# Performance work log

Measured on AMD Instinct MI355X. Metric: run time of the kernel, lower is better.

Reference implementation:

```python
import jax, jax.numpy as jnp
import numpy as np

B, L, D = 2048, 64, 128
NODES = 512
EPS = 1e-6


def setup_inputs() -> dict:
    key = jax.random.key(0)
    ks = jax.random.split(key, 9)
    src_ids = jax.random.randint(ks[0], (B, L), 0, NODES, dtype=jnp.int32)
    dst_ids = jax.random.randint(ks[1], (B, L), 0, NODES, dtype=jnp.int32)
    src_node_ids = jax.random.randint(ks[2], (B,), 1, NODES, dtype=jnp.int32)
    dst_node_ids = jax.random.randint(ks[3], (B,), 1, NODES, dtype=jnp.int32)
    node_interact_times = 100.0 + jax.random.uniform(ks[4], (B,), jnp.float32)
    src_times = jax.random.uniform(ks[5], (B, L), jnp.float32) * 100.0
    dst_times = jax.random.uniform(ks[6], (B, L), jnp.float32) * 100.0
    W1 = jax.random.normal(ks[7], (1, D), jnp.float32) * 0.5
    b1 = jnp.zeros((D,), jnp.float32)
    W2 = jax.random.normal(ks[8], (D, D), jnp.float32) * (1.0 / np.sqrt(D))
    b2 = jnp.zeros((D,), jnp.float32)
    return dict(src_padded_nodes_neighbor_ids=src_ids,
                dst_padded_nodes_neighbor_ids=dst_ids,
                src_node_ids=src_node_ids, dst_node_ids=dst_node_ids,
                node_interact_times=node_interact_times,
                src_padded_nodes_neighbor_times=src_times,
                dst_padded_nodes_neighbor_times=dst_times,
                W1=W1, b1=b1, W2=W2, b2=b2)


def _group_stats(ids, t):
    # per-position stats of the group sharing the same neighbor id. ids,t: (L,)
    n_pos = ids.shape[0]
    eq = ids[:, None] == ids[None, :]                       # (L,L) group membership
    n = eq.sum(1)                                           # group size at each position
    nf = n.astype(t.dtype)
    tb = jnp.broadcast_to(t[None, :], (n_pos, n_pos))
    tmax = jnp.max(jnp.where(eq, tb, -jnp.inf), axis=1)
    tmin = jnp.min(jnp.where(eq, tb, jnp.inf), axis=1)
    # mean(diff(sorted(ts))) == (max-min)/(n-1)
    avg_iat = jnp.where(n > 1, (tmax - tmin) / jnp.maximum(nf - 1.0, 1.0), 0.0)
    # stable rank of each element inside its own group (order statistic)
    pos = jnp.arange(n_pos)
    before = (t[:, None] < t[None, :]) | ((t[:, None] == t[None, :]) & (pos[:, None] < pos[None, :]))
    rank = jnp.sum(eq & before, axis=0)
    split = n // 2
    sel = eq & (rank[None, :] == split[:, None])            # exactly one per group
    t_split = jnp.sum(jnp.where(sel, tb, 0.0), axis=1)      # sorted(ts)[n//2]
    denom = jnp.maximum(nf - split.astype(t.dtype) - 1.0, 1.0)
    recent_iat = jnp.where(n >= 4, (tmax - t_split) / denom, 0.0)
    valid = ids != 0                                        # dicts skip neighbor id 0
    return nf, jnp.where(valid, avg_iat, 0.0), jnp.where(valid, recent_iat, 0.0)


def _cross_lookup(ids_a, ids_b, vals_b):
    # dict.get(nid, 0.0) over the other side's per-group values (id 0 excluded)
    match = (ids_a[:, None] == ids_b[None, :]) & (ids_b[None, :] != 0)
    idx = jnp.argmax(match, axis=1)
    return jnp.where(match.any(1), vals_b[idx], 0.0)


def _last_time(ids_a, ids_b, t_b):
    # dict comprehension keeps the LAST occurrence's timestamp (id 0 excluded)
    match = (ids_a[:, None] == ids_b[None, :]) & (ids_b[None, :] != 0)
    score = jnp.where(match, jnp.arange(ids_b.shape[0])[None, :], -1)
    li = score.max(1)
    return jnp.where(li >= 0, t_b[jnp.maximum(li, 0)], 0.0)


def _side_features(ids_a, t_a, ids_b, t_b, other_node_id, cur_t,
                   n_a, avg_a, rec_a, avg_b, rec_b, other_first):
    ft = t_a.dtype
    c_self = n_a
    c_other = jnp.sum(ids_a[:, None] == ids_b[None, :], axis=1).astype(ft)
    is_other = (ids_a == other_node_id).astype(ft)
    connects = (c_other > 0).astype(ft)
    freq_asym = jnp.where(c_other > 0, c_self / (c_other + EPS), 0.0)
    rcy_self = cur_t - t_a
    rcy_other = cur_t - _last_time(ids_a, ids_b, t_b)
    temp_asym = jnp.where(rcy_self > EPS, rcy_other / (rcy_self + EPS), 0.0)
    iat_other = _cross_lookup(ids_a, ids_b, avg_b)
    iat_asym = jnp.where(iat_other > EPS, avg_a / (iat_other + EPS), 0.0)
    riat_other = _cross_lookup(ids_a, ids_b, rec_b)
    riat_asym = jnp.where(riat_other > EPS, rec_a / (riat_other + EPS), 0.0)
    if other_first:
        head = [c_other, c_self]
    else:
        head = [c_self, c_other]
    return jnp.stack(head + [is_other, connects, freq_asym, temp_asym, iat_asym, riat_asym], axis=1)


def _per_sample(ids_s, ids_d, sid, did, cur_t, t_s, t_d):
    n_s, avg_s, rec_s = _group_stats(ids_s, t_s)
    n_d, avg_d, rec_d = _group_stats(ids_d, t_d)
    f_src = _side_features(ids_s, t_s, ids_d, t_d, did, cur_t,
                           n_s, avg_s, rec_s, avg_d, rec_d, False)
    f_dst = _side_features(ids_d, t_d, ids_s, t_s, sid, cur_t,
                           n_d, avg_d, rec_d, avg_s, rec_s, True)
    return f_src, f_dst


def _mlp_sum(feats, W1, b1, W2, b2):
    # Linear(1->D) -> ReLU -> Linear(D->D), applied per scalar feature, summed over the 8 features
    h = jax.nn.relu(feats[..., None] * W1[0] + b1)           # [B,L,8,D]
    y = jnp.einsum('blfd,de->blfe', h, W2) + b2
    return y.sum(axis=2)                                      # [B,L,D]


def reference(src_padded_nodes_neighbor_ids, dst_padded_nodes_neighbor_ids,
              src_node_ids, dst_node_ids, node_interact_times,
              src_padded_nodes_neighbor_times, dst_padded_nodes_neighbor_times,
              W1, b1, W2, b2):
    f_src, f_dst = jax.vmap(_per_sample)(
        src_padded_nodes_neighbor_ids, dst_padded_nodes_neighbor_ids,
        src_node_ids, dst_node_ids, node_interact_times,
        src_padded_nodes_neighbor_times, dst_padded_nodes_neighbor_times)
    f_src = jnp.where((src_padded_nodes_neighbor_ids == 0)[..., None], 0.0, f_src)
    f_dst = jnp.where((dst_padded_nodes_neighbor_ids == 0)[..., None], 0.0, f_dst)
    src_path_features = _mlp_sum(f_src, W1, b1, W2, b2)
    dst_path_features = _mlp_sum(f_dst, W1, b1, W2, b2)
    return src_path_features, dst_path_features
```

## Files before the change

kernel.cpp:

```cpp
#include <hip/hip_runtime.h>


#define EPSF 1e-6f
#define LDB 136

typedef __attribute__((ext_vector_type(8))) short bf16x8;
typedef __attribute__((ext_vector_type(4))) float f32x4;
typedef __attribute__((ext_vector_type(2))) float f32x2;

__device__ inline short f2bf(float x) {
    unsigned u = __float_as_uint(x);
    return (short)((u + 0x7fffu + ((u >> 16) & 1u)) >> 16);
}

__global__ void w2t_prep(const float* __restrict__ W2, short* __restrict__ w2t) {
    const int idx = blockIdx.x * 256 + threadIdx.x;
    const int k = idx >> 7, n = idx & 127;
    w2t[n * 128 + k] = f2bf(W2[idx]);
}

template <bool FROMWS>
__launch_bounds__(256, 4)
__global__ void lpe_fused1(const int* __restrict__ src_ids,
                           const int* __restrict__ dst_ids,
                           const int* __restrict__ src_nid,
                           const int* __restrict__ dst_nid,
                           const float* __restrict__ t_now,
                           const float* __restrict__ src_t,
                           const float* __restrict__ dst_t,
                           const float* __restrict__ W1,
                           const float* __restrict__ b1,
                           const float* __restrict__ W2,
                           const float* __restrict__ b2,
                           const short* __restrict__ w2t,
                           float* __restrict__ out)
{
    __shared__ int2  s_idt[128];
    __shared__ f32x4 s_tab[2][512];
    __shared__ float s_feats[128][9];
    __shared__ float s_w1[128], s_b1[128], s_b2[128];
    __shared__ float s_stage[4][32][32];
    __shared__ short W2T[FROMWS ? 8 : 128 * LDB];

    const int tid = threadIdx.x;
    const int b   = blockIdx.x;
    const int lane = tid & 63, wv = tid >> 6;
    const int quad = lane >> 4, ln = lane & 15;

    const float cur   = t_now[b];
    const int   src_n = src_nid[b];
    const int   dst_n = dst_nid[b];

    bf16x8 af00[4];
    if constexpr (FROMWS) {
        #pragma unroll
        for (int kk = 0; kk < 4; ++kk)
            af00[kk] = *(const bf16x8*)&w2t[ln * 128 + kk * 32 + quad * 8];
    }

    #pragma unroll
    for (int u = tid; u < 1024; u += 256) ((float*)s_tab)[u * 4] = 0.f;
    if (tid < 128) { s_w1[tid] = W1[tid]; s_b1[tid] = b1[tid]; s_b2[tid] = b2[tid]; }

    const int side = (tid >> 6) & 1;
    const int i    = tid & 63;
    int   my_id = 0;
    float my_t  = 0.f;
    if (tid < 128) {
        const int*   idp = side ? dst_ids : src_ids;
        const float* tp  = side ? dst_t   : src_t;
        my_id = idp[b * 64 + i];
        my_t  = tp [b * 64 + i];
        s_idt[tid] = make_int2(my_id, __float_as_int(my_t));
    }
    if constexpr (!FROMWS) {
        for (int u = tid; u < 16384; u += 256) {
            const int k = u >> 7, n = u & 127;
            W2T[n * LDB + k] = f2bf(W2[u]);
        }
    }
    __syncthreads();

    float nf = 0.f, avg = 0.f;
    if (tid < 128) {
        int n = 0, rank = 0, later = 0;
        float tmax = -3.4e38f, tmin = 3.4e38f;
        const int sbase = side * 64;
        #pragma unroll 8
        for (int j = 0; j < 64; ++j) {
            const int2 e = s_idt[sbase + j];
            const float tj = __int_as_float(e.y);
            if (e.x == my_id) {
                ++n;
                tmax = fmaxf(tmax, tj);
                tmin = fminf(tmin, tj);
                if (tj < my_t || (tj == my_t && j < i)) ++rank;
                if (j > i) later = 1;
            }
        }
        nf = (float)n;
        const int split = n >> 1;
        avg = (n > 1) ? (tmax - tmin) / (nf - 1.f) : 0.f;
        if (my_id != 0) {
            s_tab[side][my_id].x = nf;
            s_tab[side][my_id].y = avg;
            if (rank == split)
                s_tab[side][my_id].z = (n >= 4)
                    ? (tmax - my_t) / fmaxf(nf - (float)split - 1.f, 1.f) : 0.f;
            if (!later)
                s_tab[side][my_id].w = my_t;
        }
    }
    __syncthreads();

    if (tid < 128) {
        const int os = side ^ 1;
        const float rec_m = (my_id != 0) ? s_tab[side][my_id].z : 0.f;
        const f32x4 to = s_tab[os][my_id];
        const float n_o = (my_id != 0) ? to.x : 0.f;
        const bool  hit = n_o > 0.f;
        const float avg_o = hit ? to.y : 0.f;
        const float rec_o = hit ? to.z : 0.f;
        const float lastt = hit ? to.w : 0.f;
        const int other_node = side ? src_n : dst_n;
        const float m = (my_id != 0) ? 1.f : 0.f;

        const float rcy_s = cur - my_t;
        const float rcy_o = cur - lastt;
        s_feats[tid][0] = m * nf;
        s_feats[tid][1] = m * n_o;
        s_feats[tid][2] = m * ((my_id == other_node) ? 1.f : 0.f);
        s_feats[tid][3] = m * (hit ? 1.f : 0.f);
        s_feats[tid][4] = m * (hit ? nf / (n_o + EPSF) : 0.f);
        s_feats[tid][5] = m * ((rcy_s > EPSF) ? rcy_o / (rcy_s + EPSF) : 0.f);
        s_feats[tid][6] = m * ((avg_o > EPSF) ? avg / (avg_o + EPSF) : 0.f);
        s_feats[tid][7] = m * ((rec_o > EPSF) ? rec_m / (rec_o + EPSF) : 0.f);
    }
    __syncthreads();

    float fxr[2][8];
    #pragma unroll
    for (int rg = 0; rg < 2; ++rg) {
        const int row = wv * 32 + rg * 16 + ln;
        #pragma unroll
        for (int j = 0; j < 8; ++j) fxr[rg][j] = s_feats[row][j];
    }

    bf16x8 gf[2][4];
    #pragma unroll
    for (int kk = 0; kk < 4; ++kk) {
        const int kb = kk * 32 + quad * 8;
        #pragma unroll
        for (int rg = 0; rg < 2; ++rg) {
            #pragma unroll
            for (int u2 = 0; u2 < 4; ++u2) {
                const f32x2 w  = *(const f32x2*)&s_w1[kb + u2 * 2];
                const f32x2 bb = *(const f32x2*)&s_b1[kb + u2 * 2];
                f32x2 s = {0.f, 0.f};
                #pragma unroll
                for (int f = 0; f < 8; ++f) {
                    const f32x2 h = w * fxr[rg][f] + bb;
                    s += __builtin_elementwise_max(h, (f32x2){0.f, 0.f});
                }
                gf[rg][kk][u2 * 2]     = f2bf(s.x);
                gf[rg][kk][u2 * 2 + 1] = f2bf(s.y);
            }
        }
    }

    const long side_stride = 2048L * 64L * 128L;
    const long rowbase = (long)b * 64;
    float* st = &s_stage[wv][0][0];
    const int sw = ln & 7;

    #pragma unroll
    for (int p = 0; p < 4; ++p) {
        const int et0 = 2 * p, et1 = 2 * p + 1;
        bf16x8 afA[4], afB[4];
        #pragma unroll
        for (int kk = 0; kk < 4; ++kk) {
            if constexpr (FROMWS) {
                afA[kk] = (p == 0) ? af00[kk]
                        : *(const bf16x8*)&w2t[(et0 * 16 + ln) * 128 + kk * 32 + quad * 8];
                afB[kk] = *(const bf16x8*)&w2t[(et1 * 16 + ln) * 128 + kk * 32 + quad * 8];
            } else {
                afA[kk] = *(const bf16x8*)&W2T[(et0 * 16 + ln) * LDB + kk * 32 + quad * 8];
                afB[kk] = *(const bf16x8*)&W2T[(et1 * 16 + ln) * LDB + kk * 32 + quad * 8];
            }
        }
        f32x4 accA[2] = {(f32x4){0.f,0.f,0.f,0.f}, (f32x4){0.f,0.f,0.f,0.f}};
        f32x4 accB[2] = {(f32x4){0.f,0.f,0.f,0.f}, (f32x4){0.f,0.f,0.f,0.f}};
        #pragma unroll
        for (int kk = 0; kk < 4; ++kk)
            #pragma unroll
            for (int rg = 0; rg < 2; ++rg) {
                accA[rg] = __builtin_amdgcn_mfma_f32_16x16x32_bf16(afA[kk], gf[rg][kk], accA[rg], 0, 0, 0);
                accB[rg] = __builtin_amdgcn_mfma_f32_16x16x32_bf16(afB[kk], gf[rg][kk], accB[rg], 0, 0, 0);
            }
        const f32x4 bA = *(const f32x4*)&s_b2[et0 * 16 + quad * 4] * 8.f;
        const f32x4 bB = *(const f32x4*)&s_b2[et1 * 16 + quad * 4] * 8.f;

        if (p)
            asm volatile("s_waitcnt lgkmcnt(0)" ::: "memory");
        #pragma unroll
        for (int rg = 0; rg < 2; ++rg) {
            const int row = rg * 16 + ln;
            *(f32x4*)&st[row * 32 + ((quad ^ sw) * 4)]       = accA[rg] + bA;
            *(f32x4*)&st[row * 32 + (((4 + quad) ^ sw) * 4)] = accB[rg] + bB;
        }
        asm volatile("s_waitcnt lgkmcnt(0)" ::: "memory");
        #pragma unroll
        for (int rr = 0; rr < 4; ++rr) {
            const int rl = rr * 8 + (lane >> 3);
            const f32x4 v = *(const f32x4*)&st[rl * 32 + (((lane & 7) ^ (rl & 7)) * 4)];
            const int row = wv * 32 + rl;
            const int sd = row >> 6, ii = row & 63;
            __builtin_nontemporal_store(v,
                (f32x4*)&out[(long)sd * side_stride + (rowbase + ii) * 128
                             + p * 32 + (lane & 7) * 4]);
        }
    }
}

extern "C" void kernel_launch(void* const* d_in, const int* in_sizes, int n_in,
                              void* d_out, int out_size, void* d_ws, size_t ws_size,
                              hipStream_t stream) {
    (void)in_sizes; (void)n_in; (void)out_size;
    const int*   src_ids = (const int*)  d_in[0];
    const int*   dst_ids = (const int*)  d_in[1];
    const int*   src_nid = (const int*)  d_in[2];
    const int*   dst_nid = (const int*)  d_in[3];
    const float* t_now   = (const float*)d_in[4];
    const float* src_t   = (const float*)d_in[5];
    const float* dst_t   = (const float*)d_in[6];
    const float* W1      = (const float*)d_in[7];
    const float* b1      = (const float*)d_in[8];
    const float* W2      = (const float*)d_in[9];
    const float* b2      = (const float*)d_in[10];
    float* out = (float*)d_out;

    if (ws_size >= (size_t)(128 * 128 * 2)) {
        short* w2t = (short*)d_ws;
        w2t_prep<<<64, 256, 0, stream>>>(W2, w2t);
        lpe_fused1<true><<<2048, 256, 0, stream>>>(src_ids, dst_ids, src_nid, dst_nid,
                                                   t_now, src_t, dst_t, W1, b1, W2, b2,
                                                   w2t, out);
    } else {
        lpe_fused1<false><<<2048, 256, 0, stream>>>(src_ids, dst_ids, src_nid, dst_nid,
                                                    t_now, src_t, dst_t, W1, b1, W2, b2,
                                                    nullptr, out);
    }
}
```

Measured before the change: 193.3 us.

## Process four samples per block, staging bf16 W2 in LDS once

Each block now handles four batch samples instead of one, loading and transposing W2 into LDS once per block and reusing it across the samples. The separate W2 prep kernel and workspace path are gone. Next-sample ids and times are prefetched during the group-stats phase. The grid shrinks to 512 blocks with launch bounds allowing two blocks per CU and a larger LDS footprint, which may reduce parallelism and latency hiding.

Result: slower. 203.4 us (+5.2%).

```diff
diff --git a/kernel.cpp b/kernel.cpp
--- a/kernel.cpp
+++ b/kernel.cpp
@@ -13,15 +13,8 @@
     return (short)((u + 0x7fffu + ((u >> 16) & 1u)) >> 16);
 }
 
-__global__ void w2t_prep(const float* __restrict__ W2, short* __restrict__ w2t) {
-    const int idx = blockIdx.x * 256 + threadIdx.x;
-    const int k = idx >> 7, n = idx & 127;
-    w2t[n * 128 + k] = f2bf(W2[idx]);
-}
-
-template <bool FROMWS>
-__launch_bounds__(256, 4)
-__global__ void lpe_fused1(const int* __restrict__ src_ids,
+__launch_bounds__(256, 2)
+__global__ void lpe_fused4(const int* __restrict__ src_ids,
                            const int* __restrict__ dst_ids,
                            const int* __restrict__ src_nid,
                            const int* __restrict__ dst_nid,
@@ -32,192 +25,188 @@
                            const float* __restrict__ b1,
                            const float* __restrict__ W2,
                            const float* __restrict__ b2,
-                           const short* __restrict__ w2t,
                            float* __restrict__ out)
 {
     __shared__ int2  s_idt[128];
-    __shared__ f32x4 s_tab[2][512];
+    __shared__ __align__(16) f32x4 s_tab[2][512];
     __shared__ float s_feats[128][9];
-    __shared__ float s_w1[128], s_b1[128], s_b2[128];
-    __shared__ float s_stage[4][32][32];
-    __shared__ short W2T[FROMWS ? 8 : 128 * LDB];
-
-    const int tid = threadIdx.x;
-    const int b   = blockIdx.x;
+    __shared__ __align__(16) float s_w1[128], s_b1[128], s_b2[128];
+    __shared__ __align__(16) float s_stage[4][32][32];
+    __shared__ __align__(16) short W2T[128 * LDB];
+
+    const int tid  = threadIdx.x;
+    const int b4   = blockIdx.x * 4;
     const int lane = tid & 63, wv = tid >> 6;
     const int quad = lane >> 4, ln = lane & 15;
-
-    const float cur   = t_now[b];
-    const int   src_n = src_nid[b];
-    const int   dst_n = dst_nid[b];
-
-    bf16x8 af00[4];
-    if constexpr (FROMWS) {
-        #pragma unroll
-        for (int kk = 0; kk < 4; ++kk)
-            af00[kk] = *(const bf16x8*)&w2t[ln * 128 + kk * 32 + quad * 8];
-    }
-
-    #pragma unroll
-    for (int u = tid; u < 1024; u += 256) ((float*)s_tab)[u * 4] = 0.f;
-    if (tid < 128) { s_w1[tid] = W1[tid]; s_b1[tid] = b1[tid]; s_b2[tid] = b2[tid]; }
-
     const int side = (tid >> 6) & 1;
     const int i    = tid & 63;
-    int   my_id = 0;
-    float my_t  = 0.f;
-    if (tid < 128) {
-        const int*   idp = side ? dst_ids : src_ids;
-        const float* tp  = side ? dst_t   : src_t;
-        my_id = idp[b * 64 + i];
-        my_t  = tp [b * 64 + i];
-        s_idt[tid] = make_int2(my_id, __float_as_int(my_t));
+
+    if (tid < 128) { s_w1[tid] = W1[tid]; s_b1[tid] = b1[tid]; s_b2[tid] = b2[tid]; }
+    for (int u = tid; u < 16384; u += 256) {
+        const int k = u >> 7, n = u & 127;
+        W2T[n * LDB + k] = f2bf(W2[u]);
     }
-    if constexpr (!FROMWS) {
-        for (int u = tid; u < 16384; u += 256) {
-            const int k = u >> 7, n = u & 127;
-            W2T[n * LDB + k] = f2bf(W2[u]);
-        }
-    }
-    __syncthreads();
-
-    float nf = 0.f, avg = 0.f;
-    if (tid < 128) {
-        int n = 0, rank = 0, later = 0;
-        float tmax = -3.4e38f, tmin = 3.4e38f;
-        const int sbase = side * 64;
-        #pragma unroll 8
-        for (int j = 0; j < 64; ++j) {
-            const int2 e = s_idt[sbase + j];
-            const float tj = __int_as_float(e.y);
-            if (e.x == my_id) {
-                ++n;
-                tmax = fmaxf(tmax, tj);
-                tmin = fminf(tmin, tj);
-                if (tj < my_t || (tj == my_t && j < i)) ++rank;
-                if (j > i) later = 1;
-            }
-        }
-        nf = (float)n;
-        const int split = n >> 1;
-        avg = (n > 1) ? (tmax - tmin) / (nf - 1.f) : 0.f;
-        if (my_id != 0) {
-            s_tab[side][my_id].x = nf;
-            s_tab[side][my_id].y = avg;
-            if (rank == split)
-                s_tab[side][my_id].z = (n >= 4)
-                    ? (tmax - my_t) / fmaxf(nf - (float)split - 1.f, 1.f) : 0.f;
-            if (!later)
-                s_tab[side][my_id].w = my_t;
-        }
-    }
-    __syncthreads();
-
-    if (tid < 128) {
-        const int os = side ^ 1;
-        const float rec_m = (my_id != 0) ? s_tab[side][my_id].z : 0.f;
-        const f32x4 to = s_tab[os][my_id];
-        const float n_o = (my_id != 0) ? to.x : 0.f;
-        const bool  hit = n_o > 0.f;
-        const float avg_o = hit ? to.y : 0.f;
-        const float rec_o = hit ? to.z : 0.f;
-        const float lastt = hit ? to.w : 0.f;
-        const int other_node = side ? src_n : dst_n;
-        const float m = (my_id != 0) ? 1.f : 0.f;
-
-        const float rcy_s = cur - my_t;
-        const float rcy_o = cur - lastt;
-        s_feats[tid][0] = m * nf;
-        s_feats[tid][1] = m * n_o;
-        s_feats[tid][2] = m * ((my_id == other_node) ? 1.f : 0.f);
-        s_feats[tid][3] = m * (hit ? 1.f : 0.f);
-        s_feats[tid][4] = m * (hit ? nf / (n_o + EPSF) : 0.f);
-        s_feats[tid][5] = m * ((rcy_s > EPSF) ? rcy_o / (rcy_s + EPSF) : 0.f);
-        s_feats[tid][6] = m * ((avg_o > EPSF) ? avg / (avg_o + EPSF) : 0.f);
-        s_feats[tid][7] = m * ((rec_o > EPSF) ? rec_m / (rec_o + EPSF) : 0.f);
-    }
-    __syncthreads();
-
-    float fxr[2][8];
-    #pragma unroll
-    for (int rg = 0; rg < 2; ++rg) {
-        const int row = wv * 32 + rg * 16 + ln;
-        #pragma unroll
-        for (int j = 0; j < 8; ++j) fxr[rg][j] = s_feats[row][j];
-    }
-
-    bf16x8 gf[2][4];
-    #pragma unroll
-    for (int kk = 0; kk < 4; ++kk) {
-        const int kb = kk * 32 + quad * 8;
+
+    const int*   idp = side ? dst_ids : src_ids;
+    const float* tp  = side ? dst_t   : src_t;
+
+    int   pf_id = 0; float pf_t = 0.f;
+    if (tid < 128) { pf_id = idp[b4 * 64 + i]; pf_t = tp[b4 * 64 + i]; }
+    float cur = t_now[b4];
+    int   s_n = src_nid[b4], d_n = dst_nid[b4];
+
+    for (int u = tid; u < 1024; u += 256) ((float*)s_tab)[u * 4] = 0.f;
+
+    const long side_stride = 2048L * 64L * 128L;
+
+    for (int s = 0; s < 4; ++s) {
+        const int   my_id = pf_id;  const float my_t = pf_t;
+        const float curs  = cur;    const int sns = s_n, dns = d_n;
+        if (tid < 128) s_idt[tid] = make_int2(my_id, __float_as_int(my_t));
+        __syncthreads();
+
+        float nf = 0.f, avg = 0.f;
+        if (tid < 128) {
+            int n = 0, rank = 0, later = 0;
+            float tmax = -3.4e38f, tmin = 3.4e38f;
+            const int sbase = side * 64;
+            #pragma unroll 8
+            for (int j = 0; j < 64; ++j) {
+                const int2 e = s_idt[sbase + j];
+                const float tj = __int_as_float(e.y);
+                if (e.x == my_id) {
+                    ++n;
+                    tmax = fmaxf(tmax, tj);
+                    tmin = fminf(tmin, tj);
+                    if (tj < my_t || (tj == my_t && j < i)) ++rank;
+                    if (j > i) later = 1;
+                }
+            }
+            nf = (float)n;
+            const int split = n >> 1;
+            avg = (n > 1) ? (tmax - tmin) / (nf - 1.f) : 0.f;
+            if (my_id != 0) {
+                s_tab[side][my_id].x = nf;
+                s_tab[side][my_id].y = avg;
+                if (rank == split)
+                    s_tab[side][my_id].z = (n >= 4)
+                        ? (tmax - my_t) / fmaxf(nf - (float)split - 1.f, 1.f) : 0.f;
+                if (!later)
+                    s_tab[side][my_id].w = my_t;
+            }
+        }
+        if (s < 3) {
+            if (tid < 128) {
+                pf_id = idp[(b4 + s + 1) * 64 + i];
+                pf_t  = tp [(b4 + s + 1) * 64 + i];
+            }
+            cur = t_now[b4 + s + 1];
+            s_n = src_nid[b4 + s + 1];
+            d_n = dst_nid[b4 + s + 1];
+        }
+        __syncthreads();
+
+        if (tid < 128) {
+            const int os = side ^ 1;
+            const float rec_m = (my_id != 0) ? s_tab[side][my_id].z : 0.f;
+            const f32x4 to = s_tab[os][my_id];
+            const float n_o = (my_id != 0) ? to.x : 0.f;
+            const bool  hit = n_o > 0.f;
+            const float avg_o = hit ? to.y : 0.f;
+            const float rec_o = hit ? to.z : 0.f;
+            const float lastt = hit ? to.w : 0.f;
+            const int other_node = side ? sns : dns;
+            const float m = (my_id != 0) ? 1.f : 0.f;
+
+            const float rcy_s = curs - my_t;
+            const float rcy_o = curs - lastt;
+            s_feats[tid][0] = m * nf;
+            s_feats[tid][1] = m * n_o;
+            s_feats[tid][2] = m * ((my_id == other_node) ? 1.f : 0.f);
+            s_feats[tid][3] = m * (hit ? 1.f : 0.f);
+            s_feats[tid][4] = m * (hit ? nf / (n_o + EPSF) : 0.f);
+            s_feats[tid][5] = m * ((rcy_s > EPSF) ? rcy_o / (rcy_s + EPSF) : 0.f);
+            s_feats[tid][6] = m * ((avg_o > EPSF) ? avg / (avg_o + EPSF) : 0.f);
+            s_feats[tid][7] = m * ((rec_o > EPSF) ? rec_m / (rec_o + EPSF) : 0.f);
+        }
+        __syncthreads();
+
+        float fxr[2][8];
         #pragma unroll
         for (int rg = 0; rg < 2; ++rg) {
-            #pragma unroll
-            for (int u2 = 0; u2 < 4; ++u2) {
-                const f32x2 w  = *(const f32x2*)&s_w1[kb + u2 * 2];
-                const f32x2 bb = *(const f32x2*)&s_b1[kb + u2 * 2];
-                f32x2 s = {0.f, 0.f};
-                #pragma unroll
-                for (int f = 0; f < 8; ++f) {
-                    const f32x2 h = w * fxr[rg][f] + bb;
-                    s += __builtin_elementwise_max(h, (f32x2){0.f, 0.f});
-                }
-                gf[rg][kk][u2 * 2]     = f2bf(s.x);
-                gf[rg][kk][u2 * 2 + 1] = f2bf(s.y);
-            }
-        }
-    }
-
-    const long side_stride = 2048L * 64L * 128L;
-    const long rowbase = (long)b * 64;
-    float* st = &s_stage[wv][0][0];
-    const int sw = ln & 7;
-
-    #pragma unroll
-    for (int p = 0; p < 4; ++p) {
-        const int et0 = 2 * p, et1 = 2 * p + 1;
-        bf16x8 afA[4], afB[4];
+            const int row = wv * 32 + rg * 16 + ln;
+            #pragma unroll
+            for (int j = 0; j < 8; ++j) fxr[rg][j] = s_feats[row][j];
+        }
+        if (s < 3)
+            for (int u = tid; u < 1024; u += 256) ((float*)s_tab)[u * 4] = 0.f;
+
+        bf16x8 gf[2][4];
         #pragma unroll
         for (int kk = 0; kk < 4; ++kk) {
-            if constexpr (FROMWS) {
-                afA[kk] = (p == 0) ? af00[kk]
-                        : *(const bf16x8*)&w2t[(et0 * 16 + ln) * 128 + kk * 32 + quad * 8];
-                afB[kk] = *(const bf16x8*)&w2t[(et1 * 16 + ln) * 128 + kk * 32 + quad * 8];
-            } else {
+            const int kb = kk * 32 + quad * 8;
+            #pragma unroll
+            for (int rg = 0; rg < 2; ++rg) {
+                #pragma unroll
+                for (int u2 = 0; u2 < 4; ++u2) {
+                    const f32x2 w  = *(const f32x2*)&s_w1[kb + u2 * 2];
+                    const f32x2 bb = *(const f32x2*)&s_b1[kb + u2 * 2];
+                    f32x2 sv = {0.f, 0.f};
+                    #pragma unroll
+                    for (int f = 0; f < 8; ++f) {
+                        const f32x2 h = w * fxr[rg][f] + bb;
+                        sv += __builtin_elementwise_max(h, (f32x2){0.f, 0.f});
+                    }
+                    gf[rg][kk][u2 * 2]     = f2bf(sv.x);
+                    gf[rg][kk][u2 * 2 + 1] = f2bf(sv.y);
+                }
+            }
+        }
+
+        float* st = &s_stage[wv][0][0];
+        const int sw = ln & 7;
+        const long rowbase = (long)(b4 + s) * 64;
+
+        #pragma unroll
+        for (int p = 0; p < 4; ++p) {
+            const int et0 = 2 * p, et1 = 2 * p + 1;
+            bf16x8 afA[4], afB[4];
+            #pragma unroll
+            for (int kk = 0; kk < 4; ++kk) {
                 afA[kk] = *(const bf16x8*)&W2T[(et0 * 16 + ln) * LDB + kk * 32 + quad * 8];
                 afB[kk] = *(const bf16x8*)&W2T[(et1 * 16 + ln) * LDB + kk * 32 + quad * 8];
             }
-        }
-        f32x4 accA[2] = {(f32x4){0.f,0.f,0.f,0.f}, (f32x4){0.f,0.f,0.f,0.f}};
-        f32x4 accB[2] = {(f32x4){0.f,0.f,0.f,0.f}, (f32x4){0.f,0.f,0.f,0.f}};
-        #pragma unroll
-        for (int kk = 0; kk < 4; ++kk)
+            f32x4 accA[2] = {(f32x4){0.f,0.f,0.f,0.f}, (f32x4){0.f,0.f,0.f,0.f}};
+            f32x4 accB[2] = {(f32x4){0.f,0.f,0.f,0.f}, (f32x4){0.f,0.f,0.f,0.f}};
+            #pragma unroll
+            for (int kk = 0; kk < 4; ++kk)
+                #pragma unroll
+                for (int rg = 0; rg < 2; ++rg) {
+                    accA[rg] = __builtin_amdgcn_mfma_f32_16x16x32_bf16(afA[kk], gf[rg][kk], accA[rg], 0, 0, 0);
+                    accB[rg] = __builtin_amdgcn_mfma_f32_16x16x32_bf16(afB[kk], gf[rg][kk], accB[rg], 0, 0, 0);
+                }
+            const f32x4 bA = *(const f32x4*)&s_b2[et0 * 16 + quad * 4] * 8.f;
+            const f32x4 bB = *(const f32x4*)&s_b2[et1 * 16 + quad * 4] * 8.f;
+
+            if (p)
+                asm volatile("s_waitcnt lgkmcnt(0)" ::: "memory");
             #pragma unroll
             for (int rg = 0; rg < 2; ++rg) {
-                accA[rg] = __builtin_amdgcn_mfma_f32_16x16x32_bf16(afA[kk], gf[rg][kk], accA[rg], 0, 0, 0);
-                accB[rg] = __builtin_amdgcn_mfma_f32_16x16x32_bf16(afB[kk], gf[rg][kk], accB[rg], 0, 0, 0);
-            }
-        const f32x4 bA = *(const f32x4*)&s_b2[et0 * 16 + quad * 4] * 8.f;
-        const f32x4 bB = *(const f32x4*)&s_b2[et1 * 16 + quad * 4] * 8.f;
-
-        if (p)
+                const int row = rg * 16 + ln;
+                *(f32x4*)&st[row * 32 + ((quad ^ sw) * 4)]       = accA[rg] + bA;
+                *(f32x4*)&st[row * 32 + (((4 + quad) ^ sw) * 4)] = accB[rg] + bB;
+            }
             asm volatile("s_waitcnt lgkmcnt(0)" ::: "memory");
-        #pragma unroll
-        for (int rg = 0; rg < 2; ++rg) {
-            const int row = rg * 16 + ln;
-            *(f32x4*)&st[row * 32 + ((quad ^ sw) * 4)]       = accA[rg] + bA;
-            *(f32x4*)&st[row * 32 + (((4 + quad) ^ sw) * 4)] = accB[rg] + bB;
-        }
-        asm volatile("s_waitcnt lgkmcnt(0)" ::: "memory");
-        #pragma unroll
-        for (int rr = 0; rr < 4; ++rr) {
-            const int rl = rr * 8 + (lane >> 3);
-            const f32x4 v = *(const f32x4*)&st[rl * 32 + (((lane & 7) ^ (rl & 7)) * 4)];
-            const int row = wv * 32 + rl;
-            const int sd = row >> 6, ii = row & 63;
-            __builtin_nontemporal_store(v,
-                (f32x4*)&out[(long)sd * side_stride + (rowbase + ii) * 128
-                             + p * 32 + (lane & 7) * 4]);
+            #pragma unroll
+            for (int rr = 0; rr < 4; ++rr) {
+                const int rl = rr * 8 + (lane >> 3);
+                const f32x4 v = *(const f32x4*)&st[rl * 32 + (((lane & 7) ^ (rl & 7)) * 4)];
+                const int row = wv * 32 + rl;
+                const int sd = row >> 6, ii = row & 63;
+                __builtin_nontemporal_store(v,
+                    (f32x4*)&out[(long)sd * side_stride + (rowbase + ii) * 128
+                                 + p * 32 + (lane & 7) * 4]);
+            }
         }
     }
 }
@@ -225,7 +214,7 @@
 extern "C" void kernel_launch(void* const* d_in, const int* in_sizes, int n_in,
                               void* d_out, int out_size, void* d_ws, size_t ws_size,
                               hipStream_t stream) {
-    (void)in_sizes; (void)n_in; (void)out_size;
+    (void)in_sizes; (void)n_in; (void)out_size; (void)d_ws; (void)ws_size;
     const int*   src_ids = (const int*)  d_in[0];
     const int*   dst_ids = (const int*)  d_in[1];
     const int*   src_nid = (const int*)  d_in[2];
@@ -239,15 +228,6 @@
     const float* b2      = (const float*)d_in[10];
     float* out = (float*)d_out;
 
-    if (ws_size >= (size_t)(128 * 128 * 2)) {
-        short* w2t = (short*)d_ws;
-        w2t_prep<<<64, 256, 0, stream>>>(W2, w2t);
-        lpe_fused1<true><<<2048, 256, 0, stream>>>(src_ids, dst_ids, src_nid, dst_nid,
-                                                   t_now, src_t, dst_t, W1, b1, W2, b2,
-                                                   w2t, out);
-    } else {
-        lpe_fused1<false><<<2048, 256, 0, stream>>>(src_ids, dst_ids, src_nid, dst_nid,
-                                                    t_now, src_t, dst_t, W1, b1, W2, b2,
-                                                    nullptr, out);
-    }
+    lpe_fused4<<<512, 256, 0, stream>>>(src_ids, dst_ids, src_nid, dst_nid,
+                                        t_now, src_t, dst_t, W1, b1, W2, b2, out);
 }
```
